# Performance work log

Hardware: AMD Instinct MI355X
Metric: run time of the kernel (lower is better)

## Reference

```python
import jax, jax.numpy as jnp
import numpy as np

# Geometry / discretization constants (mirrors WaveCell.__init__)
NX, NY = 192, 192
DT = 1e-3
CMAX = 1.0
H = DT * CMAX * np.sqrt(2.0) * 1.01  # auto-set h as in __init__ (satisfies CFL)
SRC_X, SRC_Y = 96, 32  # point source grid location


def _laplacian(y, inv_h2):
    # y: [B, Nx, Ny]; 5-point stencil with zero padding (conv2d padding=1)
    p = jnp.pad(y, ((0, 0), (1, 1), (1, 1)))
    return inv_h2 * (p[:, :-2, 1:-1] + p[:, 2:, 1:-1]
                     + p[:, 1:-1, :-2] + p[:, 1:-1, 2:] - 4.0 * y)


def setup_inputs() -> dict:
    key = jax.random.key(0)
    k1, k2, k3 = jax.random.split(key, 3)
    B, T = 4, 256
    x = jax.random.normal(k1, (B, T, 1), dtype=jnp.float32)
    # per-cell wave speed in [0,1) so cmax <= 1 (CFL-safe)
    c = jax.random.uniform(k2, (NX, NY), dtype=jnp.float32)
    # boundary absorber damping coefficient
    b = jax.random.uniform(k3, (NX, NY), dtype=jnp.float32)
    return {"x": x, "c": c, "b": b}


def reference(x, c, b):
    B, T = x.shape[0], x.shape[1]
    inv_h2 = 1.0 / (H * H)
    inv_dt2 = 1.0 / (DT * DT)
    a_inv = 1.0 / (inv_dt2 + 0.5 * b / DT)   # [Nx, Ny]
    coef2 = inv_dt2 - 0.5 * b / DT           # [Nx, Ny]
    c2 = c * c

    x_seq = jnp.transpose(x[..., 0], (1, 0))  # [T, B]

    def step(carry, xt):
        y1, y2 = carry  # fields one and two steps ago
        y = a_inv * (2.0 * inv_dt2 * y1 - coef2 * y2 + c2 * _laplacian(y1, inv_h2))
        y = y.at[:, SRC_X, SRC_Y].add(xt)  # point source injection
        return (y, y1), y

    y0 = jnp.zeros((B, NX, NY), dtype=x.dtype)
    _, ys = jax.lax.scan(step, (y0, y0), x_seq)  # ys: [T, B, Nx, Ny]
    return jnp.transpose(ys, (1, 0, 2, 3))       # [B, T, Nx, Ny]
```

## Files before the change

### kernel.cpp

```cpp
#include <hip/hip_runtime.h>


#define NXg 192
#define NYg 192
#define BATCH 4
#define TSTEPS 256
#define CELLS (NXg * NYg)

#define TS 24
#define KSTEP 16
#define EXT 56
#define LROWS (EXT + 2)
#define LPITCH 68
#define LSZ (LROWS * LPITCH)
#define NTHREADS 448

#define SRC_X 96
#define SRC_Y 32

__global__ __launch_bounds__(NTHREADS) void wave_tile_kernel(
    const float* __restrict__ cgp, const float* __restrict__ bgp,
    const float* __restrict__ x, float* __restrict__ out, int t0) {
  __shared__ float buf0[LSZ];
  __shared__ float buf1[LSZ];

  const int tid = threadIdx.x;
  const int lr = tid >> 3;
  const int lg = tid & 7;
  const int bcol = blockIdx.x;
  const int brow = blockIdx.y;
  const int bb = blockIdx.z;
  const int r0 = brow * TS - KSTEP;
  const int c0 = bcol * TS - KSTEP;
  const int obase = bb * TSTEPS * CELLS;
  const float inv_h2 = (float)(1.0 / (2.0 * 1.01 * 1.01 * 1.0e-3 * 1.0e-3));

  const int gr = r0 + lr;
  const int gc = c0 + 8 * lg;
  const bool id = (lg < 7) && (gr >= 0) && (gr < NXg) && (gc >= 0) && (gc < NYg);
  const bool til = (lr >= KSTEP) && (lr < KSTEP + TS) && (lg >= 2) && (lg < 5);
  const int gofs = id ? (gr * NYg + gc) : 0;

  const float4 z4 = make_float4(0.f, 0.f, 0.f, 0.f);

  float4 cv0 = z4, cv1 = z4, bv0 = z4, bv1 = z4;
  float4 yc0 = z4, yc1 = z4, yp0 = z4, yp1 = z4;
  if (id) {
    cv0 = *(const float4*)(cgp + gofs);
    cv1 = *(const float4*)(cgp + gofs + 4);
    bv0 = *(const float4*)(bgp + gofs);
    bv1 = *(const float4*)(bgp + gofs + 4);
    if (t0 > 0) {
      yc0 = *(const float4*)(out + obase + (t0 - 1) * CELLS + gofs);
      yc1 = *(const float4*)(out + obase + (t0 - 1) * CELLS + gofs + 4);
      yp0 = *(const float4*)(out + obase + (t0 - 2) * CELLS + gofs);
      yp1 = *(const float4*)(out + obase + (t0 - 2) * CELLS + gofs + 4);
    }
  }
  float xs[KSTEP];
  {
    const float4* xp = (const float4*)(x + bb * TSTEPS + t0);
    float4 a0 = xp[0], a1 = xp[1], a2 = xp[2], a3 = xp[3];
    xs[0] = a0.x; xs[1] = a0.y; xs[2] = a0.z; xs[3] = a0.w;
    xs[4] = a1.x; xs[5] = a1.y; xs[6] = a1.z; xs[7] = a1.w;
    xs[8] = a2.x; xs[9] = a2.y; xs[10] = a2.z; xs[11] = a2.w;
    xs[12] = a3.x; xs[13] = a3.y; xs[14] = a3.z; xs[15] = a3.w;
  }

  if (tid < 64) {
    const int sel = tid >> 4;
    const int g = tid & 15;
    float* base = (sel & 2) ? buf1 : buf0;
    const int row = (sel & 1) ? (LROWS - 1) : 0;
    *(float4*)&base[row * LPITCH + 4 + 4 * g] = z4;
  }

  float4 ai0 = z4, ai1 = z4, cf0 = z4, cf1 = z4, cs0 = z4, cs1 = z4;
  float4 sm0 = z4, sm1 = z4;
  if (id) {
    ai0.x = 1.0f / (1.0e6f + 500.0f * bv0.x);
    ai0.y = 1.0f / (1.0e6f + 500.0f * bv0.y);
    ai0.z = 1.0f / (1.0e6f + 500.0f * bv0.z);
    ai0.w = 1.0f / (1.0e6f + 500.0f * bv0.w);
    ai1.x = 1.0f / (1.0e6f + 500.0f * bv1.x);
    ai1.y = 1.0f / (1.0e6f + 500.0f * bv1.y);
    ai1.z = 1.0f / (1.0e6f + 500.0f * bv1.z);
    ai1.w = 1.0f / (1.0e6f + 500.0f * bv1.w);
    cf0.x = 1.0e6f - 500.0f * bv0.x;
    cf0.y = 1.0e6f - 500.0f * bv0.y;
    cf0.z = 1.0e6f - 500.0f * bv0.z;
    cf0.w = 1.0e6f - 500.0f * bv0.w;
    cf1.x = 1.0e6f - 500.0f * bv1.x;
    cf1.y = 1.0e6f - 500.0f * bv1.y;
    cf1.z = 1.0e6f - 500.0f * bv1.z;
    cf1.w = 1.0e6f - 500.0f * bv1.w;
    cs0.x = cv0.x * cv0.x; cs0.y = cv0.y * cv0.y;
    cs0.z = cv0.z * cv0.z; cs0.w = cv0.w * cv0.w;
    cs1.x = cv1.x * cv1.x; cs1.y = cv1.y * cv1.y;
    cs1.z = cv1.z * cv1.z; cs1.w = cv1.w * cv1.w;
    if (gr == SRC_X) {
      sm0.x = (gc + 0 == SRC_Y) ? 1.0f : 0.0f;
      sm0.y = (gc + 1 == SRC_Y) ? 1.0f : 0.0f;
      sm0.z = (gc + 2 == SRC_Y) ? 1.0f : 0.0f;
      sm0.w = (gc + 3 == SRC_Y) ? 1.0f : 0.0f;
      sm1.x = (gc + 4 == SRC_Y) ? 1.0f : 0.0f;
      sm1.y = (gc + 5 == SRC_Y) ? 1.0f : 0.0f;
      sm1.z = (gc + 6 == SRC_Y) ? 1.0f : 0.0f;
      sm1.w = (gc + 7 == SRC_Y) ? 1.0f : 0.0f;
    }
  }

  const int lo = (lr + 1) * LPITCH + 4 + 8 * lg;
  *(float4*)&buf0[lo] = yc0;
  *(float4*)&buf0[lo + 4] = yc1;
  __syncthreads();

  float* ping = buf0;
  float* pong = buf1;

  float4 pv0 = z4, pv1 = z4;
  float* pop = out;

#pragma unroll
  for (int j = 0; j < KSTEP; ++j) {
    const float xt = xs[j];
    float* op = out + obase + (t0 + j) * CELLS;

    if (j > 0 && til) {
      *(float4*)(pop + gofs) = pv0;
      *(float4*)(pop + gofs + 4) = pv1;
    }

    float lqw = __shfl_up(yc1.w, 1);
    lqw = (lg == 0) ? 0.0f : lqw;
    float rqx = __shfl_down(yc0.x, 1);

    float4 up0 = *(float4*)&ping[lo - LPITCH];
    float4 up1 = *(float4*)&ping[lo - LPITCH + 4];
    float4 dn0 = *(float4*)&ping[lo + LPITCH];
    float4 dn1 = *(float4*)&ping[lo + LPITCH + 4];

    float4 val0, val1;
    {
      float lap = inv_h2 * (up0.x + dn0.x + lqw + yc0.y - 4.0f * yc0.x);
      val0.x = ai0.x * (2.0e6f * yc0.x - cf0.x * yp0.x + cs0.x * lap) + sm0.x * xt;
    }
    {
      float lap = inv_h2 * (up0.y + dn0.y + yc0.x + yc0.z - 4.0f * yc0.y);
      val0.y = ai0.y * (2.0e6f * yc0.y - cf0.y * yp0.y + cs0.y * lap) + sm0.y * xt;
    }
    {
      float lap = inv_h2 * (up0.z + dn0.z + yc0.y + yc0.w - 4.0f * yc0.z);
      val0.z = ai0.z * (2.0e6f * yc0.z - cf0.z * yp0.z + cs0.z * lap) + sm0.z * xt;
    }
    {
      float lap = inv_h2 * (up0.w + dn0.w + yc0.z + yc1.x - 4.0f * yc0.w);
      val0.w = ai0.w * (2.0e6f * yc0.w - cf0.w * yp0.w + cs0.w * lap) + sm0.w * xt;
    }
    {
      float lap = inv_h2 * (up1.x + dn1.x + yc0.w + yc1.y - 4.0f * yc1.x);
      val1.x = ai1.x * (2.0e6f * yc1.x - cf1.x * yp1.x + cs1.x * lap) + sm1.x * xt;
    }
    {
      float lap = inv_h2 * (up1.y + dn1.y + yc1.x + yc1.z - 4.0f * yc1.y);
      val1.y = ai1.y * (2.0e6f * yc1.y - cf1.y * yp1.y + cs1.y * lap) + sm1.y * xt;
    }
    {
      float lap = inv_h2 * (up1.z + dn1.z + yc1.y + yc1.w - 4.0f * yc1.z);
      val1.z = ai1.z * (2.0e6f * yc1.z - cf1.z * yp1.z + cs1.z * lap) + sm1.z * xt;
    }
    {
      float lap = inv_h2 * (up1.w + dn1.w + yc1.z + rqx - 4.0f * yc1.w);
      val1.w = ai1.w * (2.0e6f * yc1.w - cf1.w * yp1.w + cs1.w * lap) + sm1.w * xt;
    }

    yp0 = yc0; yp1 = yc1;
    yc0 = val0; yc1 = val1;

    *(float4*)&pong[lo] = val0;
    *(float4*)&pong[lo + 4] = val1;

    pv0 = val0; pv1 = val1; pop = op;

    __syncthreads();
    float* tmp = ping; ping = pong; pong = tmp;
  }

  if (til) {
    *(float4*)(pop + gofs) = pv0;
    *(float4*)(pop + gofs + 4) = pv1;
  }
}

extern "C" void kernel_launch(void* const* d_in, const int* in_sizes, int n_in,
                              void* d_out, int out_size, void* d_ws,
                              size_t ws_size, hipStream_t stream) {
  const float* x = (const float*)d_in[0];
  const float* c = (const float*)d_in[1];
  const float* b = (const float*)d_in[2];
  float* out = (float*)d_out;

  dim3 grid(NXg / TS, NYg / TS, BATCH);
  for (int t0 = 0; t0 < TSTEPS; t0 += KSTEP) {
    wave_tile_kernel<<<grid, NTHREADS, 0, stream>>>(c, b, x, out, t0);
  }
}
```

Before: 321.0 us.

## Skip dead halo rows per step and fold stencil coefficients into FMAs

Each time step now updates only the rows that can still yield a valid result. The valid region shrinks by one row per side each step, so threads outside it skip their shared-memory loads and arithmetic. The per-cell update is rewritten with precomputed combined coefficients (2/dt² scaled by a_inv, the damping term scaled by a_inv, and c²·inv_h2·a_inv), which removes the per-step multiplies and the shared-memory zeroing of the boundary rows. Source injection runs only in blocks that contain the source. The row skip diverges at 8-lane granularity, so whole waves only drop out in later steps, and the coefficient folding changes rounding slightly.

```diff
diff --git a/kernel.cpp b/kernel.cpp
--- a/kernel.cpp
+++ b/kernel.cpp
@@ -39,6 +39,8 @@
   const int gc = c0 + 8 * lg;
   const bool id = (lg < 7) && (gr >= 0) && (gr < NXg) && (gc >= 0) && (gc < NYg);
   const bool til = (lr >= KSTEP) && (lr < KSTEP + TS) && (lg >= 2) && (lg < 5);
+  const bool hs = (SRC_X >= r0) && (SRC_X < r0 + EXT) &&
+                  (SRC_Y >= c0) && (SRC_Y < c0 + EXT);
   const int gofs = id ? (gr * NYg + gc) : 0;
 
   const float4 z4 = make_float4(0.f, 0.f, 0.f, 0.f);
@@ -67,37 +69,34 @@
     xs[12] = a3.x; xs[13] = a3.y; xs[14] = a3.z; xs[15] = a3.w;
   }
 
-  if (tid < 64) {
-    const int sel = tid >> 4;
-    const int g = tid & 15;
-    float* base = (sel & 2) ? buf1 : buf0;
-    const int row = (sel & 1) ? (LROWS - 1) : 0;
-    *(float4*)&base[row * LPITCH + 4 + 4 * g] = z4;
-  }
-
-  float4 ai0 = z4, ai1 = z4, cf0 = z4, cf1 = z4, cs0 = z4, cs1 = z4;
+  float4 Dc0 = z4, Dc1 = z4, Ey0 = z4, Ey1 = z4, G0 = z4, G1 = z4;
   float4 sm0 = z4, sm1 = z4;
   if (id) {
-    ai0.x = 1.0f / (1.0e6f + 500.0f * bv0.x);
-    ai0.y = 1.0f / (1.0e6f + 500.0f * bv0.y);
-    ai0.z = 1.0f / (1.0e6f + 500.0f * bv0.z);
-    ai0.w = 1.0f / (1.0e6f + 500.0f * bv0.w);
-    ai1.x = 1.0f / (1.0e6f + 500.0f * bv1.x);
-    ai1.y = 1.0f / (1.0e6f + 500.0f * bv1.y);
-    ai1.z = 1.0f / (1.0e6f + 500.0f * bv1.z);
-    ai1.w = 1.0f / (1.0e6f + 500.0f * bv1.w);
-    cf0.x = 1.0e6f - 500.0f * bv0.x;
-    cf0.y = 1.0e6f - 500.0f * bv0.y;
-    cf0.z = 1.0e6f - 500.0f * bv0.z;
-    cf0.w = 1.0e6f - 500.0f * bv0.w;
-    cf1.x = 1.0e6f - 500.0f * bv1.x;
-    cf1.y = 1.0e6f - 500.0f * bv1.y;
-    cf1.z = 1.0e6f - 500.0f * bv1.z;
-    cf1.w = 1.0e6f - 500.0f * bv1.w;
-    cs0.x = cv0.x * cv0.x; cs0.y = cv0.y * cv0.y;
-    cs0.z = cv0.z * cv0.z; cs0.w = cv0.w * cv0.w;
-    cs1.x = cv1.x * cv1.x; cs1.y = cv1.y * cv1.y;
-    cs1.z = cv1.z * cv1.z; cs1.w = cv1.w * cv1.w;
+    float ai;
+    ai = 1.0f / (1.0e6f + 500.0f * bv0.x);
+    Dc0.x = 2.0e6f * ai; Ey0.x = (1.0e6f - 500.0f * bv0.x) * ai;
+    G0.x = (cv0.x * cv0.x) * inv_h2 * ai;
+    ai = 1.0f / (1.0e6f + 500.0f * bv0.y);
+    Dc0.y = 2.0e6f * ai; Ey0.y = (1.0e6f - 500.0f * bv0.y) * ai;
+    G0.y = (cv0.y * cv0.y) * inv_h2 * ai;
+    ai = 1.0f / (1.0e6f + 500.0f * bv0.z);
+    Dc0.z = 2.0e6f * ai; Ey0.z = (1.0e6f - 500.0f * bv0.z) * ai;
+    G0.z = (cv0.z * cv0.z) * inv_h2 * ai;
+    ai = 1.0f / (1.0e6f + 500.0f * bv0.w);
+    Dc0.w = 2.0e6f * ai; Ey0.w = (1.0e6f - 500.0f * bv0.w) * ai;
+    G0.w = (cv0.w * cv0.w) * inv_h2 * ai;
+    ai = 1.0f / (1.0e6f + 500.0f * bv1.x);
+    Dc1.x = 2.0e6f * ai; Ey1.x = (1.0e6f - 500.0f * bv1.x) * ai;
+    G1.x = (cv1.x * cv1.x) * inv_h2 * ai;
+    ai = 1.0f / (1.0e6f + 500.0f * bv1.y);
+    Dc1.y = 2.0e6f * ai; Ey1.y = (1.0e6f - 500.0f * bv1.y) * ai;
+    G1.y = (cv1.y * cv1.y) * inv_h2 * ai;
+    ai = 1.0f / (1.0e6f + 500.0f * bv1.z);
+    Dc1.z = 2.0e6f * ai; Ey1.z = (1.0e6f - 500.0f * bv1.z) * ai;
+    G1.z = (cv1.z * cv1.z) * inv_h2 * ai;
+    ai = 1.0f / (1.0e6f + 500.0f * bv1.w);
+    Dc1.w = 2.0e6f * ai; Ey1.w = (1.0e6f - 500.0f * bv1.w) * ai;
+    G1.w = (cv1.w * cv1.w) * inv_h2 * ai;
     if (gr == SRC_X) {
       sm0.x = (gc + 0 == SRC_Y) ? 1.0f : 0.0f;
       sm0.y = (gc + 1 == SRC_Y) ? 1.0f : 0.0f;
@@ -121,6 +120,12 @@
   float4 pv0 = z4, pv1 = z4;
   float* pop = out;
 
+#define CELL(dst, up_, dn_, lf_, rt_, D_, E_, Gc_, y_, p_)              \
+  {                                                                     \
+    float s_ = fmaf(-4.0f, y_, (up_ + dn_) + (lf_ + rt_));              \
+    dst = fmaf(Gc_, s_, fmaf(-E_, p_, D_ * y_));                        \
+  }
+
 #pragma unroll
   for (int j = 0; j < KSTEP; ++j) {
     const float xt = xs[j];
@@ -131,60 +136,53 @@
       *(float4*)(pop + gofs + 4) = pv1;
     }
 
-    float lqw = __shfl_up(yc1.w, 1);
-    lqw = (lg == 0) ? 0.0f : lqw;
-    float rqx = __shfl_down(yc0.x, 1);
-
-    float4 up0 = *(float4*)&ping[lo - LPITCH];
-    float4 up1 = *(float4*)&ping[lo - LPITCH + 4];
-    float4 dn0 = *(float4*)&ping[lo + LPITCH];
-    float4 dn1 = *(float4*)&ping[lo + LPITCH + 4];
-
-    float4 val0, val1;
-    {
-      float lap = inv_h2 * (up0.x + dn0.x + lqw + yc0.y - 4.0f * yc0.x);
-      val0.x = ai0.x * (2.0e6f * yc0.x - cf0.x * yp0.x + cs0.x * lap) + sm0.x * xt;
-    }
-    {
-      float lap = inv_h2 * (up0.y + dn0.y + yc0.x + yc0.z - 4.0f * yc0.y);
-      val0.y = ai0.y * (2.0e6f * yc0.y - cf0.y * yp0.y + cs0.y * lap) + sm0.y * xt;
-    }
-    {
-      float lap = inv_h2 * (up0.z + dn0.z + yc0.y + yc0.w - 4.0f * yc0.z);
-      val0.z = ai0.z * (2.0e6f * yc0.z - cf0.z * yp0.z + cs0.z * lap) + sm0.z * xt;
-    }
-    {
-      float lap = inv_h2 * (up0.w + dn0.w + yc0.z + yc1.x - 4.0f * yc0.w);
-      val0.w = ai0.w * (2.0e6f * yc0.w - cf0.w * yp0.w + cs0.w * lap) + sm0.w * xt;
-    }
-    {
-      float lap = inv_h2 * (up1.x + dn1.x + yc0.w + yc1.y - 4.0f * yc1.x);
-      val1.x = ai1.x * (2.0e6f * yc1.x - cf1.x * yp1.x + cs1.x * lap) + sm1.x * xt;
-    }
-    {
-      float lap = inv_h2 * (up1.y + dn1.y + yc1.x + yc1.z - 4.0f * yc1.y);
-      val1.y = ai1.y * (2.0e6f * yc1.y - cf1.y * yp1.y + cs1.y * lap) + sm1.y * xt;
-    }
-    {
-      float lap = inv_h2 * (up1.z + dn1.z + yc1.y + yc1.w - 4.0f * yc1.z);
-      val1.z = ai1.z * (2.0e6f * yc1.z - cf1.z * yp1.z + cs1.z * lap) + sm1.z * xt;
-    }
-    {
-      float lap = inv_h2 * (up1.w + dn1.w + yc1.z + rqx - 4.0f * yc1.w);
-      val1.w = ai1.w * (2.0e6f * yc1.w - cf1.w * yp1.w + cs1.w * lap) + sm1.w * xt;
-    }
-
-    yp0 = yc0; yp1 = yc1;
-    yc0 = val0; yc1 = val1;
-
-    *(float4*)&pong[lo] = val0;
-    *(float4*)&pong[lo + 4] = val1;
-
-    pv0 = val0; pv1 = val1; pop = op;
+    const bool alive = (lr >= j + 1) && (lr <= 54 - j);
+    if (alive) {
+      float lqw = __shfl_up(yc1.w, 1);
+      lqw = (lg == 0) ? 0.0f : lqw;
+      float rqx = __shfl_down(yc0.x, 1);
+      rqx = (lg == 7) ? 0.0f : rqx;
+
+      float4 up0 = *(float4*)&ping[lo - LPITCH];
+      float4 up1 = *(float4*)&ping[lo - LPITCH + 4];
+      float4 dn0 = *(float4*)&ping[lo + LPITCH];
+      float4 dn1 = *(float4*)&ping[lo + LPITCH + 4];
+
+      float4 val0, val1;
+      CELL(val0.x, up0.x, dn0.x, lqw,    yc0.y, Dc0.x, Ey0.x, G0.x, yc0.x, yp0.x);
+      CELL(val0.y, up0.y, dn0.y, yc0.x,  yc0.z, Dc0.y, Ey0.y, G0.y, yc0.y, yp0.y);
+      CELL(val0.z, up0.z, dn0.z, yc0.y,  yc0.w, Dc0.z, Ey0.z, G0.z, yc0.z, yp0.z);
+      CELL(val0.w, up0.w, dn0.w, yc0.z,  yc1.x, Dc0.w, Ey0.w, G0.w, yc0.w, yp0.w);
+      CELL(val1.x, up1.x, dn1.x, yc0.w,  yc1.y, Dc1.x, Ey1.x, G1.x, yc1.x, yp1.x);
+      CELL(val1.y, up1.y, dn1.y, yc1.x,  yc1.z, Dc1.y, Ey1.y, G1.y, yc1.y, yp1.y);
+      CELL(val1.z, up1.z, dn1.z, yc1.y,  yc1.w, Dc1.z, Ey1.z, G1.z, yc1.z, yp1.z);
+      CELL(val1.w, up1.w, dn1.w, yc1.z,  rqx,   Dc1.w, Ey1.w, G1.w, yc1.w, yp1.w);
+
+      if (hs) {
+        val0.x = fmaf(sm0.x, xt, val0.x);
+        val0.y = fmaf(sm0.y, xt, val0.y);
+        val0.z = fmaf(sm0.z, xt, val0.z);
+        val0.w = fmaf(sm0.w, xt, val0.w);
+        val1.x = fmaf(sm1.x, xt, val1.x);
+        val1.y = fmaf(sm1.y, xt, val1.y);
+        val1.z = fmaf(sm1.z, xt, val1.z);
+        val1.w = fmaf(sm1.w, xt, val1.w);
+      }
+
+      yp0 = yc0; yp1 = yc1;
+      yc0 = val0; yc1 = val1;
+
+      *(float4*)&pong[lo] = val0;
+      *(float4*)&pong[lo + 4] = val1;
+
+      pv0 = val0; pv1 = val1;
+    }
+    pop = op;
 
     __syncthreads();
     float* tmp = ping; ping = pong; pong = tmp;
   }
+#undef CELL
 
   if (til) {
     *(float4*)(pop + gofs) = pv0;
```

New measurement: 324.2 us. No clear change (+1.0%).
